# Performance work log

Hardware: AMD Instinct MI355X
Metric: run time of the kernel (lower is better)

## Reference

```python
import jax, jax.numpy as jnp
import numpy as np

H = 12  # num_attention_heads

def setup_inputs() -> dict:
    key = jax.random.key(0)
    ks = jax.random.split(key, 6)
    B, S, D = 2, 2048, 768
    sc = 0.02
    return {
        "hidden_states": jax.random.normal(ks[0], (B, S, D), jnp.float32),
        "Wqr": jax.random.normal(ks[1], (D, D), jnp.float32) * sc,
        "Wqi": jax.random.normal(ks[2], (D, D), jnp.float32) * sc,
        "Wkr": jax.random.normal(ks[3], (D, D), jnp.float32) * sc,
        "Wki": jax.random.normal(ks[4], (D, D), jnp.float32) * sc,
        "Wv": jax.random.normal(ks[5], (D, D), jnp.float32) * sc,
    }

def _heads(x, B, S):
    # [B,S,D] -> [B,H,S,Dh]
    return x.reshape(B, S, H, -1).transpose(0, 2, 1, 3)

def reference(hidden_states, Wqr, Wqi, Wkr, Wki, Wv):
    B, S, D = hidden_states.shape
    Dh = D // H
    x = hidden_states  # real input; imag part is zero
    # complex projections with zero imag input: q = (x@Wqr.T) + i (x@Wqi.T), same for k
    qr = _heads(x @ Wqr.T, B, S)
    qi = _heads(x @ Wqi.T, B, S)
    kr = _heads(x @ Wkr.T, B, S)
    ki = _heads(x @ Wki.T, B, S)
    v = _heads(x @ Wv.T, B, S)
    scale = 1.0 / jnp.sqrt(jnp.float32(Dh))
    # complex QK^H in real arithmetic: s = q @ conj(k)^T
    sr = (jnp.einsum('bhqd,bhkd->bhqk', qr, kr) +
          jnp.einsum('bhqd,bhkd->bhqk', qi, ki)) * scale
    si = (jnp.einsum('bhqd,bhkd->bhqk', qi, kr) -
          jnp.einsum('bhqd,bhkd->bhqk', qr, ki)) * scale
    scores = jnp.sqrt(sr * sr + si * si)  # 'magnitude' variant
    probs = jax.nn.softmax(scores, axis=-1)
    ctx = jnp.einsum('bhqk,bhkd->bhqd', probs, v)
    return ctx.transpose(0, 2, 1, 3).reshape(B, S, D)
```

## Files before the change

kernel.cpp:

```cpp
#include <hip/hip_runtime.h>
#include <cstdint>

typedef short bf16x8 __attribute__((ext_vector_type(8)));
typedef float f32x4 __attribute__((ext_vector_type(4)));

#define MFMA16(a, b, c) __builtin_amdgcn_mfma_f32_16x16x32_bf16((a), (b), (c), 0, 0, 0)

__device__ __forceinline__ unsigned short f2b(float f) {
  union { float f; unsigned int u; } x; x.f = f;
  unsigned int r = x.u + 0x7fffu + ((x.u >> 16) & 1u);
  return (unsigned short)(r >> 16);
}

__device__ __forceinline__ unsigned int pack2(float lo, float hi) {
  union { float f; unsigned int u; } a, b;
  a.f = lo; b.f = hi;
  return ((a.u + 0x8000u) >> 16) | ((b.u + 0x8000u) & 0xffff0000u);
}

#define NB 2
#define NS 2048
#define ND 768
#define NH 12
#define DHD 64
#define MTOK 4096

#define OFF_XB 0
#define OFF_WB 3145728
#define OFF_QK 6094848
#define OFF_VT 18677760

__global__ void cvt_kernel(const float* __restrict__ src,
                           unsigned short* __restrict__ dst, int n4, float scale) {
  int i = blockIdx.x * blockDim.x + threadIdx.x;
  if (i >= n4) return;
  float4 v = ((const float4*)src)[i];
  ushort4 o;
  o.x = f2b(v.x * scale); o.y = f2b(v.y * scale);
  o.z = f2b(v.z * scale); o.w = f2b(v.w * scale);
  ((ushort4*)dst)[i] = o;
}

__global__ __launch_bounds__(256) void proj_kernel(
    const unsigned short* __restrict__ Xb, const unsigned short* __restrict__ Wb,
    unsigned short* __restrict__ QK, unsigned short* __restrict__ Vt) {
  __shared__ __align__(16) unsigned short S[18432];
  unsigned short* Xs = S;
  unsigned short* Ws = S + 9216;

  const int lin = blockIdx.x + 6 * (blockIdx.y + 5 * blockIdx.z);
  const int sb = (lin & 7) * 120 + (lin >> 3);
  const int n0 = (sb % 6) * 128;
  const int rem = sb / 6;
  const int z = rem % 5;
  const int m0 = (rem / 5) * 128;

  const unsigned short* Wz = Wb + z * 589824;
  const int tid = threadIdx.x;
  const int lane = tid & 63;
  const int w = tid >> 6;
  const int wm = (w >> 1) * 64;
  const int wn = (w & 1) * 64;
  const int col = lane & 15, quad = lane >> 4;

  f32x4 acc[4][4] = {};

  for (int k0 = 0; k0 < ND; k0 += 64) {
    __syncthreads();
#pragma unroll
    for (int i = 0; i < 4; i++) {
      int idx = tid + i * 256;
      int r = idx >> 3, c8 = (idx & 7) * 8;
      *(uint4*)(Xs + r * 72 + c8) = *(const uint4*)(Xb + (m0 + r) * ND + k0 + c8);
      *(uint4*)(Ws + r * 72 + c8) = *(const uint4*)(Wz + (n0 + r) * ND + k0 + c8);
    }
    __syncthreads();
#pragma unroll
    for (int ks = 0; ks < 2; ks++) {
      bf16x8 af[4], bw[4];
#pragma unroll
      for (int t = 0; t < 4; t++) {
        af[t] = *(const bf16x8*)(Xs + (wm + t * 16 + col) * 72 + ks * 32 + quad * 8);
        bw[t] = *(const bf16x8*)(Ws + (wn + t * 16 + col) * 72 + ks * 32 + quad * 8);
      }
#pragma unroll
      for (int mt = 0; mt < 4; mt++)
#pragma unroll
        for (int nt = 0; nt < 4; nt++)
          acc[mt][nt] = MFMA16(af[mt], bw[nt], acc[mt][nt]);
    }
  }

  __syncthreads();
  unsigned short* T = S;

  if (z < 4) {
#pragma unroll
    for (int mt = 0; mt < 4; mt++) {
      int rl = wm + mt * 16 + quad * 4;
#pragma unroll
      for (int nt = 0; nt < 4; nt++) {
        int cl = wn + nt * 16 + col;
#pragma unroll
        for (int r = 0; r < 4; r++) T[(rl + r) * 136 + cl] = f2b(acc[mt][nt][r]);
      }
    }
    __syncthreads();
    unsigned short* out = QK + z * (MTOK * ND);
    const int rr = tid >> 4;
    const int cc = (tid & 15) * 8;
#pragma unroll
    for (int p = 0; p < 8; p++) {
      int row = p * 16 + rr;
      uint4 v = *(const uint4*)(T + row * 136 + cc);
      *(uint4*)(out + (m0 + row) * ND + n0 + cc) = v;
    }
  } else {
#pragma unroll
    for (int mt = 0; mt < 4; mt++) {
      int rl = wm + mt * 16 + quad * 4;
#pragma unroll
      for (int nt = 0; nt < 4; nt++) {
        int cl = wn + nt * 16 + col;
        ushort4 pk;
        pk.x = f2b(acc[mt][nt][0]);
        pk.y = f2b(acc[mt][nt][1]);
        pk.z = f2b(acc[mt][nt][2]);
        pk.w = f2b(acc[mt][nt][3]);
        *(ushort4*)(T + cl * 136 + rl) = pk;
      }
    }
    __syncthreads();
    const int rr = tid >> 4;
    const int cc = (tid & 15) * 8;
    const int b = m0 >> 11;
    const int s_base = m0 & 2047;
#pragma unroll
    for (int p = 0; p < 8; p++) {
      int dhl = p * 16 + rr;
      int c = n0 + dhl;
      int h = c >> 6, dh = c & 63;
      uint4 v = *(const uint4*)(T + dhl * 136 + cc);
      *(uint4*)(Vt + (((b * NH + h) * DHD + dh) * NS + s_base + cc)) = v;
    }
  }
}

__global__ __launch_bounds__(256) void attn_kernel(
    const unsigned short* __restrict__ QK, const unsigned short* __restrict__ Vt,
    float* __restrict__ outp) {
  __shared__ __align__(16) unsigned short Krs[4096];
  __shared__ __align__(16) unsigned short Kis[4096];
  __shared__ __align__(16) unsigned short Vts[4096];
  __shared__ __align__(16) unsigned short Ps[4096];

  const int lin = blockIdx.x + 32 * (blockIdx.y + 12 * blockIdx.z);
  const int sb = (lin & 7) * 96 + (lin >> 3);
  const int qt = sb & 31;
  const int h = (sb >> 5) % 12;
  const int b = sb / 384;
  const int tid = threadIdx.x, lane = tid & 63, w = tid >> 6;
  const int col = lane & 15, quad = lane >> 4;
  const int c7 = col & 7;
  const int jb = quad ^ c7;
  const int f0 = jb * 8, f1 = (jb ^ 4) * 8;

  const unsigned short* Qr = QK;
  const unsigned short* Qi = QK + MTOK * ND;
  const unsigned short* Krp = QK + 2 * MTOK * ND;
  const unsigned short* Kip = QK + 3 * MTOK * ND;

  const int q_tok = b * NS + qt * 64 + w * 16 + col;
  const int qoff = q_tok * ND + h * DHD;

  bf16x8 qrf[2], qif[2], qrn[2];
#pragma unroll
  for (int kk = 0; kk < 2; kk++) {
    qrf[kk] = *(const bf16x8*)(Qr + qoff + kk * 32 + quad * 8);
    qif[kk] = *(const bf16x8*)(Qi + qoff + kk * 32 + quad * 8);
    qrn[kk] = qrf[kk] ^ (short)0x8000;
  }

  const int r0 = tid >> 3;
  const int j0 = tid & 7;
  const int dst0 = r0 * 64 + ((j0 ^ (r0 & 7)) * 8);

  const unsigned short* pKr = Krp + (b * NS + r0) * ND + h * DHD + j0 * 8;
  const unsigned short* pKi = Kip + (b * NS + r0) * ND + h * DHD + j0 * 8;
  const unsigned short* pV = Vt + (b * NH + h) * (DHD * NS) + r0 * NS + j0 * 8;

  unsigned short* PsW = Ps + w * 1024;

  f32x4 o[4] = {};
  float lrow = 0.f;

  for (int kt = 0; kt < 32; kt++) {
    __syncthreads();
    *(uint4*)(Krs + dst0) = *(const uint4*)pKr;
    *(uint4*)(Krs + dst0 + 2048) = *(const uint4*)(pKr + 32 * ND);
    *(uint4*)(Kis + dst0) = *(const uint4*)pKi;
    *(uint4*)(Kis + dst0 + 2048) = *(const uint4*)(pKi + 32 * ND);
    *(uint4*)(Vts + dst0) = *(const uint4*)pV;
    *(uint4*)(Vts + dst0 + 2048) = *(const uint4*)(pV + 32 * NS);
    pKr += 64 * ND;
    pKi += 64 * ND;
    pV += 64;
    __syncthreads();

#pragma unroll
    for (int mt = 0; mt < 4; mt++) {
      f32x4 sr = {}, si = {};
      const int rowb = (mt * 16 + col) * 64;
      bf16x8 kr0 = *(const bf16x8*)(Krs + rowb + f0);
      bf16x8 ki0 = *(const bf16x8*)(Kis + rowb + f0);
      bf16x8 kr1 = *(const bf16x8*)(Krs + rowb + f1);
      bf16x8 ki1 = *(const bf16x8*)(Kis + rowb + f1);
      sr = MFMA16(kr0, qrf[0], sr);
      sr = MFMA16(ki0, qif[0], sr);
      si = MFMA16(kr0, qif[0], si);
      si = MFMA16(ki0, qrn[0], si);
      sr = MFMA16(kr1, qrf[1], sr);
      sr = MFMA16(ki1, qif[1], sr);
      si = MFMA16(kr1, qif[1], si);
      si = MFMA16(ki1, qrn[1], si);

      float e0, e1, e2, e3;
      {
        float m0f = __builtin_amdgcn_sqrtf(sr[0] * sr[0] + si[0] * si[0]);
        float m1f = __builtin_amdgcn_sqrtf(sr[1] * sr[1] + si[1] * si[1]);
        float m2f = __builtin_amdgcn_sqrtf(sr[2] * sr[2] + si[2] * si[2]);
        float m3f = __builtin_amdgcn_sqrtf(sr[3] * sr[3] + si[3] * si[3]);
        e0 = __builtin_amdgcn_exp2f(m0f);
        e1 = __builtin_amdgcn_exp2f(m1f);
        e2 = __builtin_amdgcn_exp2f(m2f);
        e3 = __builtin_amdgcn_exp2f(m3f);
      }
      lrow += (e0 + e1) + (e2 + e3);
      uint2 pk;
      pk.x = pack2(e0, e1);
      pk.y = pack2(e2, e3);
      *(uint2*)(PsW + col * 64 + (((mt * 2 + (quad >> 1)) ^ c7) * 8) + (quad & 1) * 4) = pk;
    }
    asm volatile("s_waitcnt lgkmcnt(0)" ::: "memory");

    bf16x8 pb0 = *(const bf16x8*)(PsW + col * 64 + f0);
    bf16x8 pb1 = *(const bf16x8*)(PsW + col * 64 + f1);
#pragma unroll
    for (int dt = 0; dt < 4; dt++) {
      const int rowv = (dt * 16 + col) * 64;
      bf16x8 va0 = *(const bf16x8*)(Vts + rowv + f0);
      bf16x8 va1 = *(const bf16x8*)(Vts + rowv + f1);
      o[dt] = MFMA16(va0, pb0, o[dt]);
      o[dt] = MFMA16(va1, pb1, o[dt]);
    }
  }

  lrow += __shfl_xor(lrow, 16);
  lrow += __shfl_xor(lrow, 32);
  float inv_l = 1.0f / lrow;
  float* op = outp + (size_t)q_tok * ND + h * DHD;
#pragma unroll
  for (int dt = 0; dt < 4; dt++) {
    float4 v;
    v.x = o[dt][0] * inv_l;
    v.y = o[dt][1] * inv_l;
    v.z = o[dt][2] * inv_l;
    v.w = o[dt][3] * inv_l;
    *(float4*)(op + dt * 16 + quad * 4) = v;
  }
}

extern "C" void kernel_launch(void* const* d_in, const int* in_sizes, int n_in,
                              void* d_out, int out_size, void* d_ws, size_t ws_size,
                              hipStream_t stream) {
  const float* X = (const float*)d_in[0];
  unsigned short* ws = (unsigned short*)d_ws;
  unsigned short* Xb = ws + OFF_XB;
  unsigned short* Wb = ws + OFF_WB;
  unsigned short* QK = ws + OFF_QK;
  unsigned short* Vt = ws + OFF_VT;

  const float QSCALE = 0.125f * 1.44269504088896f;

  cvt_kernel<<<3072, 256, 0, stream>>>(X, Xb, 786432, 1.0f);
  for (int z = 0; z < 5; z++) {
    float sc = (z == 0 || z == 1) ? QSCALE : 1.0f;
    cvt_kernel<<<576, 256, 0, stream>>>((const float*)d_in[1 + z],
                                        Wb + z * 589824, 147456, sc);
  }

  proj_kernel<<<dim3(6, 5, 32), 256, 0, stream>>>(Xb, Wb, QK, Vt);
  attn_kernel<<<dim3(32, 12, 2), 256, 0, stream>>>(QK, Vt, (float*)d_out);
}
```

Before: 227.0 us.

## Use direct global-to-LDS loads with XOR swizzle and merge weight conversions

```diff
diff --git a/kernel.cpp b/kernel.cpp
--- a/kernel.cpp
+++ b/kernel.cpp
@@ -5,6 +5,12 @@
 typedef float f32x4 __attribute__((ext_vector_type(4)));
 
 #define MFMA16(a, b, c) __builtin_amdgcn_mfma_f32_16x16x32_bf16((a), (b), (c), 0, 0, 0)
+
+__device__ __forceinline__ void gl16(const unsigned short* g, unsigned short* l) {
+  __builtin_amdgcn_global_load_lds(
+      (const __attribute__((address_space(1))) unsigned int*)g,
+      (__attribute__((address_space(3))) unsigned int*)l, 16, 0, 0);
+}
 
 __device__ __forceinline__ unsigned short f2b(float f) {
   union { float f; unsigned int u; } x; x.f = f;
@@ -41,12 +47,27 @@
   ((ushort4*)dst)[i] = o;
 }
 
+__global__ void wcvt_kernel(const float* __restrict__ s0, const float* __restrict__ s1,
+                            const float* __restrict__ s2, const float* __restrict__ s3,
+                            const float* __restrict__ s4, unsigned short* __restrict__ dst,
+                            float qs) {
+  const int bz = blockIdx.x / 576;
+  const int i = (blockIdx.x % 576) * 256 + threadIdx.x;
+  const float* src = bz == 0 ? s0 : bz == 1 ? s1 : bz == 2 ? s2 : bz == 3 ? s3 : s4;
+  const float scale = bz < 2 ? qs : 1.0f;
+  float4 v = ((const float4*)src)[i];
+  ushort4 o;
+  o.x = f2b(v.x * scale); o.y = f2b(v.y * scale);
+  o.z = f2b(v.z * scale); o.w = f2b(v.w * scale);
+  ((ushort4*)(dst + bz * 589824))[i] = o;
+}
+
 __global__ __launch_bounds__(256) void proj_kernel(
     const unsigned short* __restrict__ Xb, const unsigned short* __restrict__ Wb,
     unsigned short* __restrict__ QK, unsigned short* __restrict__ Vt) {
-  __shared__ __align__(16) unsigned short S[18432];
+  __shared__ __align__(16) unsigned short S[17408];
   unsigned short* Xs = S;
-  unsigned short* Ws = S + 9216;
+  unsigned short* Ws = S + 8192;
 
   const int lin = blockIdx.x + 6 * (blockIdx.y + 5 * blockIdx.z);
   const int sb = (lin & 7) * 120 + (lin >> 3);
@@ -62,6 +83,14 @@
   const int wm = (w >> 1) * 64;
   const int wn = (w & 1) * 64;
   const int col = lane & 15, quad = lane >> 4;
+  const int c7 = col & 7;
+
+  const int lr = lane >> 3;
+  const int lc = (lane & 7) ^ (lr & 7);
+  const unsigned short* gX = Xb + (m0 + w * 32 + lr) * ND + lc * 8;
+  const unsigned short* gW = Wz + (n0 + w * 32 + lr) * ND + lc * 8;
+  unsigned short* lX = Xs + (w * 32) * 64;
+  unsigned short* lW = Ws + (w * 32) * 64;
 
   f32x4 acc[4][4] = {};
 
@@ -69,10 +98,8 @@
     __syncthreads();
 #pragma unroll
     for (int i = 0; i < 4; i++) {
-      int idx = tid + i * 256;
-      int r = idx >> 3, c8 = (idx & 7) * 8;
-      *(uint4*)(Xs + r * 72 + c8) = *(const uint4*)(Xb + (m0 + r) * ND + k0 + c8);
-      *(uint4*)(Ws + r * 72 + c8) = *(const uint4*)(Wz + (n0 + r) * ND + k0 + c8);
+      gl16(gX + i * (8 * ND) + k0, lX + i * (8 * 64));
+      gl16(gW + i * (8 * ND) + k0, lW + i * (8 * 64));
     }
     __syncthreads();
 #pragma unroll
@@ -80,8 +107,9 @@
       bf16x8 af[4], bw[4];
 #pragma unroll
       for (int t = 0; t < 4; t++) {
-        af[t] = *(const bf16x8*)(Xs + (wm + t * 16 + col) * 72 + ks * 32 + quad * 8);
-        bw[t] = *(const bf16x8*)(Ws + (wn + t * 16 + col) * 72 + ks * 32 + quad * 8);
+        const int fo = (((ks * 4 + quad) ^ c7) * 8);
+        af[t] = *(const bf16x8*)(Xs + (wm + t * 16 + col) * 64 + fo);
+        bw[t] = *(const bf16x8*)(Ws + (wn + t * 16 + col) * 64 + fo);
       }
 #pragma unroll
       for (int mt = 0; mt < 4; mt++)
@@ -181,13 +209,14 @@
     qrn[kk] = qrf[kk] ^ (short)0x8000;
   }
 
-  const int r0 = tid >> 3;
-  const int j0 = tid & 7;
-  const int dst0 = r0 * 64 + ((j0 ^ (r0 & 7)) * 8);
-
-  const unsigned short* pKr = Krp + (b * NS + r0) * ND + h * DHD + j0 * 8;
-  const unsigned short* pKi = Kip + (b * NS + r0) * ND + h * DHD + j0 * 8;
-  const unsigned short* pV = Vt + (b * NH + h) * (DHD * NS) + r0 * NS + j0 * 8;
+  const int lr = lane >> 3;
+  const int lc = (lane & 7) ^ (lr & 7);
+  const unsigned short* gKr = Krp + (b * NS + w * 8 + lr) * ND + h * DHD + lc * 8;
+  const unsigned short* gKi = Kip + (b * NS + w * 8 + lr) * ND + h * DHD + lc * 8;
+  const unsigned short* gV = Vt + (b * NH + h) * (DHD * NS) + (w * 8 + lr) * NS + lc * 8;
+  unsigned short* lKr = Krs + (w * 8) * 64;
+  unsigned short* lKi = Kis + (w * 8) * 64;
+  unsigned short* lV = Vts + (w * 8) * 64;
 
   unsigned short* PsW = Ps + w * 1024;
 
@@ -196,15 +225,15 @@
 
   for (int kt = 0; kt < 32; kt++) {
     __syncthreads();
-    *(uint4*)(Krs + dst0) = *(const uint4*)pKr;
-    *(uint4*)(Krs + dst0 + 2048) = *(const uint4*)(pKr + 32 * ND);
-    *(uint4*)(Kis + dst0) = *(const uint4*)pKi;
-    *(uint4*)(Kis + dst0 + 2048) = *(const uint4*)(pKi + 32 * ND);
-    *(uint4*)(Vts + dst0) = *(const uint4*)pV;
-    *(uint4*)(Vts + dst0 + 2048) = *(const uint4*)(pV + 32 * NS);
-    pKr += 64 * ND;
-    pKi += 64 * ND;
-    pV += 64;
+    gl16(gKr, lKr);
+    gl16(gKr + 32 * ND, lKr + 2048);
+    gl16(gKi, lKi);
+    gl16(gKi + 32 * ND, lKi + 2048);
+    gl16(gV, lV);
+    gl16(gV + 32 * NS, lV + 2048);
+    gKr += 64 * ND;
+    gKi += 64 * ND;
+    gV += 64;
     __syncthreads();
 
 #pragma unroll
@@ -283,11 +312,9 @@
   const float QSCALE = 0.125f * 1.44269504088896f;
 
   cvt_kernel<<<3072, 256, 0, stream>>>(X, Xb, 786432, 1.0f);
-  for (int z = 0; z < 5; z++) {
-    float sc = (z == 0 || z == 1) ? QSCALE : 1.0f;
-    cvt_kernel<<<576, 256, 0, stream>>>((const float*)d_in[1 + z],
-                                        Wb + z * 589824, 147456, sc);
-  }
+  wcvt_kernel<<<2880, 256, 0, stream>>>((const float*)d_in[1], (const float*)d_in[2],
+                                        (const float*)d_in[3], (const float*)d_in[4],
+                                        (const float*)d_in[5], Wb, QSCALE);
 
   proj_kernel<<<dim3(6, 5, 32), 256, 0, stream>>>(Xb, Wb, QK, Vt);
   attn_kernel<<<dim3(32, 12, 2), 256, 0, stream>>>(QK, Vt, (float*)d_out);
```

After: 193.3 us. 14.9% less time.
